# Kernel optimization log

Measured on AMD Instinct MI355X. Metric: run time of the kernel, lower is better.

Reference implementation:

```python
import jax, jax.numpy as jnp
import numpy as np

B, S, D, H = 4, 2048, 1024, 16
DK = D // H

def setup_inputs() -> dict:
    key = jax.random.key(0)
    ks = jax.random.split(key, 12)
    s = 1.0 / np.sqrt(D)
    inp = {
        'q': jax.random.normal(ks[0], (B, S, D), dtype=jnp.float32),
        'k': jax.random.normal(ks[1], (B, S, D), dtype=jnp.float32),
        'v': jax.random.normal(ks[2], (B, S, D), dtype=jnp.float32),
        'mask': jnp.ones((1, 1, S, S), dtype=jnp.int32),
        'w_q': jax.random.normal(ks[3], (D, D), dtype=jnp.float32) * s,
        'b_q': jax.random.normal(ks[4], (D,), dtype=jnp.float32) * s,
        'w_k': jax.random.normal(ks[5], (D, D), dtype=jnp.float32) * s,
        'b_k': jax.random.normal(ks[6], (D,), dtype=jnp.float32) * s,
        'w_v': jax.random.normal(ks[7], (D, D), dtype=jnp.float32) * s,
        'b_v': jax.random.normal(ks[8], (D,), dtype=jnp.float32) * s,
        'w_o': jax.random.normal(ks[9], (D, D), dtype=jnp.float32) * s,
        'b_o': jax.random.normal(ks[10], (D,), dtype=jnp.float32) * s,
    }
    return inp

def reference(q, k, v, mask, w_q, b_q, w_k, b_k, w_v, b_v, w_o, b_o):
    # Linear projections (torch nn.Linear: x @ W^T + b)
    query = q @ w_q.T + b_q            # [B,S,D]
    key_  = k @ w_k.T + b_k
    value = v @ w_v.T + b_v
    # split heads -> [B,H,S,DK]
    def split(x):
        return x.reshape(B, S, H, DK).transpose(0, 2, 1, 3)
    qh, kh, vh = split(query), split(key_), split(value)
    # scaled dot-product attention with full score matrix (naive, faithful)
    scores = jnp.einsum('bhqd,bhkd->bhqk', qh, kh) / jnp.sqrt(jnp.float32(DK))
    scores = jnp.where(mask == 0, jnp.float32(-1e9), scores)
    attn = jax.nn.softmax(scores, axis=-1)  # dropout p=0.0 -> identity
    out = jnp.einsum('bhqk,bhkd->bhqd', attn, vh)
    out = out.transpose(0, 2, 1, 3).reshape(B, S, D)
    return out @ w_o.T + b_o
```

## Files before the change

kernel.cpp:

```cpp
#include <hip/hip_runtime.h>
#include <hip/hip_bf16.h>

typedef __hip_bfloat16 bf16;
typedef __attribute__((ext_vector_type(8))) short bf16x8;
typedef __attribute__((ext_vector_type(4))) float f32x4;

#define GLD16(g, l) __builtin_amdgcn_global_load_lds( \
    (const __attribute__((address_space(1))) void*)(g), \
    (__attribute__((address_space(3))) void*)(l), 16, 0, 0)

__device__ __forceinline__ int xcd_swz(int bid, int cpx) {
  return (bid & 7) * cpx + (bid >> 3);
}


__global__ __launch_bounds__(256) void cvt_all_k(
    const float* __restrict__ q, const float* __restrict__ k,
    const float* __restrict__ v, const float* __restrict__ wq,
    const float* __restrict__ wk, const float* __restrict__ wv,
    const float* __restrict__ wo,
    bf16* __restrict__ qb, bf16* __restrict__ kb, bf16* __restrict__ vb,
    bf16* __restrict__ wqb, bf16* __restrict__ wkb, bf16* __restrict__ wvb,
    bf16* __restrict__ wob) {
  const int bx = blockIdx.x;
  const float* in;
  bf16* out;
  int idx;
  if (bx < 8192) { in = q; out = qb; idx = bx; }
  else if (bx < 16384) { in = k; out = kb; idx = bx - 8192; }
  else if (bx < 24576) { in = v; out = vb; idx = bx - 16384; }
  else {
    const int r = bx - 24576, sel = r >> 10;
    idx = r & 1023;
    in = sel == 0 ? wq : sel == 1 ? wk : sel == 2 ? wv : wo;
    out = sel == 0 ? wqb : sel == 1 ? wkb : sel == 2 ? wvb : wob;
  }
  long i = ((long)idx * 256 + threadIdx.x) * 4;
  float4 vv = *reinterpret_cast<const float4*>(in + i);
  struct alignas(8) B4 { bf16 a, b, c, d; } o;
  o.a = __float2bfloat16(vv.x);
  o.b = __float2bfloat16(vv.y);
  o.c = __float2bfloat16(vv.z);
  o.d = __float2bfloat16(vv.w);
  *reinterpret_cast<B4*>(out + i) = o;
}

template <int MODE>
__global__ __launch_bounds__(512) void gemm_bt_k(
    const bf16* __restrict__ A, const bf16* __restrict__ BT,
    const float* __restrict__ bias, void* __restrict__ outp) {
  __shared__ __align__(16) bf16 As[4][128 * 32];
  __shared__ __align__(16) bf16 Bs[4][128 * 32];
  const int swz = xcd_swz(blockIdx.x, 64);
  const int by = swz >> 3, bx = swz & 7;
  const int t = threadIdx.x;
  const int m0 = by * 128, n0 = bx * 128;
  const int w = t >> 6, lane = t & 63, lr = lane & 15, lg = lane >> 4;
  const int wr = (w >> 1) * 32, wc = (w & 1) * 64;
  f32x4 acc[2][4] = {};
  const int sr = t >> 2;
  const int scol = ((t & 3) ^ (sr & 3)) * 8;
  const bf16* ga = A + (long)(m0 + sr) * 1024 + scol;
  const bf16* gb = BT + (long)(n0 + sr) * 1024 + scol;
#define ISSUE_TILE(itv, buf) do { \
    const int _k = (itv) * 32; \
    GLD16(ga + _k, As[buf] + t * 8); \
    GLD16(gb + _k, Bs[buf] + t * 8); \
  } while (0)
  ISSUE_TILE(0, 0);
  ISSUE_TILE(1, 1);
  for (int it = 0; it < 32; ++it) {
    if (it < 30) {
      ISSUE_TILE(it + 2, (it + 2) & 3);
      asm volatile("s_waitcnt vmcnt(4)" ::: "memory");
    } else if (it == 30) {
      asm volatile("s_waitcnt vmcnt(2)" ::: "memory");
    } else {
      asm volatile("s_waitcnt vmcnt(0)" ::: "memory");
    }
    __builtin_amdgcn_s_barrier();
    const bf16* a_cur = As[it & 3];
    const bf16* b_cur = Bs[it & 3];
    bf16x8 af[2], bfr[4];
#pragma unroll
    for (int m = 0; m < 2; ++m) {
      const int row = wr + m * 16 + lr;
      af[m] = *(const bf16x8*)&a_cur[row * 32 + ((lg ^ (row & 3)) * 8)];
    }
#pragma unroll
    for (int n = 0; n < 4; ++n) {
      const int row = wc + n * 16 + lr;
      bfr[n] = *(const bf16x8*)&b_cur[row * 32 + ((lg ^ (row & 3)) * 8)];
    }
#pragma unroll
    for (int m = 0; m < 2; ++m)
#pragma unroll
      for (int n = 0; n < 4; ++n)
        acc[m][n] = __builtin_amdgcn_mfma_f32_16x16x32_bf16(af[m], bfr[n], acc[m][n], 0, 0, 0);
  }
#pragma unroll
  for (int n = 0; n < 4; ++n) {
    const int j = n0 + wc + n * 16 + lr;
    const float bj = bias[j];
    const int h = j >> 6, dk = j & 63;
#pragma unroll
    for (int m = 0; m < 2; ++m) {
#pragma unroll
      for (int r = 0; r < 4; ++r) {
        const int i = m0 + wr + m * 16 + lg * 4 + r;
        float vv = acc[m][n][r] + bj;
        if (MODE == 3) {
          ((float*)outp)[(long)i * 1024 + j] = vv;
        } else {
          const int b = i >> 11, s = i & 2047;
          if (MODE == 0) vv *= 0.18033688011112042f;
          const bf16 bv = __float2bfloat16(vv);
          if (MODE == 2)
            ((bf16*)outp)[((long)((b * 16 + h) * 64 + dk) << 11) + s] = bv;
          else
            ((bf16*)outp)[((long)((b * 16 + h) * 2048 + s) << 6) + dk] = bv;
        }
      }
    }
  }
#undef ISSUE_TILE
}

__global__ __launch_bounds__(512, 4) void attn_fwd_k(
    const bf16* __restrict__ Qp, const bf16* __restrict__ Kp,
    const bf16* __restrict__ Vp, bf16* __restrict__ Ao) {
  __shared__ __align__(16) bf16 QP[256 * 64];
  __shared__ __align__(16) bf16 Ks[2][64 * 64];
  __shared__ __align__(16) bf16 Vt[2][64 * 64];
  const int t = threadIdx.x;
  const int w = t >> 6, lane = t & 63, lr = lane & 15, lg = lane >> 4;
  const int swz = xcd_swz(blockIdx.x, 64);
  const int bh = swz >> 3;
  const int q0 = (swz & 7) * 256;
  const long hb = (long)bh * 2048 * 64;
  const int sr = t >> 3;
  const int scol8 = (t & 7) * 8;
  const int swcol = (((t & 7) ^ (sr & 7)) * 8);
  const int qscol = ((t & 7) ^ (sr & 7)) * 8;
#pragma unroll
  for (int i = 0; i < 4; ++i)
    GLD16(Qp + hb + (long)(q0 + i * 64 + sr) * 64 + qscol, QP + i * 4096 + t * 8);
  bf16x8 kreg = *(const bf16x8*)&Kp[hb + (long)sr * 64 + scol8];
  bf16x8 vreg = *(const bf16x8*)&Vp[hb + (long)sr * 2048 + scol8];
  *(bf16x8*)&Ks[0][sr * 64 + swcol] = kreg;
  *(bf16x8*)&Vt[0][sr * 64 + swcol] = vreg;
  __syncthreads();
  int fro0[2], fro1[2];
#pragma unroll
  for (int kk = 0; kk < 2; ++kk) {
    fro0[kk] = (w * 32 + lr) * 64 + (((kk * 4 + lg) ^ (lr & 7)) * 8);
    fro1[kk] = (w * 32 + 16 + lr) * 64 + (((kk * 4 + lg) ^ (lr & 7)) * 8);
  }
  int pwo0[4], pwo1[4];
#pragma unroll
  for (int mt = 0; mt < 4; ++mt) {
    const int cs = (((mt * 2 + (lg >> 1)) ^ (lr & 7)) * 8) + (lg & 1) * 4;
    pwo0[mt] = (w * 32 + lr) * 64 + cs;
    pwo1[mt] = (w * 32 + 16 + lr) * 64 + cs;
  }
  bf16x8 aq0[2], aq1[2];
  aq0[0] = *(const bf16x8*)&QP[fro0[0]];
  aq0[1] = *(const bf16x8*)&QP[fro0[1]];
  aq1[0] = *(const bf16x8*)&QP[fro1[0]];
  aq1[1] = *(const bf16x8*)&QP[fro1[1]];
  bf16x8 ones;
  {
    const short o1 = (short)0x3F80;
    ones = bf16x8{o1, o1, o1, o1, o1, o1, o1, o1};
  }
  f32x4 o0[4] = {}, o1[4] = {};
  f32x4 ol0 = {}, ol1 = {};
  struct alignas(8) P4 { __hip_bfloat162 a, b; };
  const f32x4 minit = {-16.f, -16.f, -16.f, -16.f};
  int cur = 0;
  for (int it = 0; it < 32; ++it) {
    if (it < 31) {
      const int kv1 = (it + 1) * 64;
      kreg = *(const bf16x8*)&Kp[hb + (long)(kv1 + sr) * 64 + scol8];
      vreg = *(const bf16x8*)&Vp[hb + (long)sr * 2048 + kv1 + scol8];
    }
    f32x4 s0[4] = {minit, minit, minit, minit};
    f32x4 s1[4] = {minit, minit, minit, minit};
    __builtin_amdgcn_s_setprio(1);
#pragma unroll
    for (int mt = 0; mt < 4; ++mt) {
      const int row = mt * 16 + lr;
#pragma unroll
      for (int kk = 0; kk < 2; ++kk) {
        bf16x8 bk = *(const bf16x8*)&Ks[cur][row * 64 + (((kk * 4 + lg) ^ (lr & 7)) * 8)];
        s0[mt] = __builtin_amdgcn_mfma_f32_16x16x32_bf16(bk, aq0[kk], s0[mt], 0, 0, 0);
        s1[mt] = __builtin_amdgcn_mfma_f32_16x16x32_bf16(bk, aq1[kk], s1[mt], 0, 0, 0);
      }
    }
    __builtin_amdgcn_s_setprio(0);
#pragma unroll
    for (int mt = 0; mt < 4; ++mt) {
      const float p0 = __builtin_amdgcn_exp2f(s0[mt][0]);
      const float p1 = __builtin_amdgcn_exp2f(s0[mt][1]);
      const float p2 = __builtin_amdgcn_exp2f(s0[mt][2]);
      const float p3 = __builtin_amdgcn_exp2f(s0[mt][3]);
      P4 pk;
      pk.a = __float22bfloat162_rn(make_float2(p0, p1));
      pk.b = __float22bfloat162_rn(make_float2(p2, p3));
      *(P4*)&QP[pwo0[mt]] = pk;
    }
#pragma unroll
    for (int mt = 0; mt < 4; ++mt) {
      const float p0 = __builtin_amdgcn_exp2f(s1[mt][0]);
      const float p1 = __builtin_amdgcn_exp2f(s1[mt][1]);
      const float p2 = __builtin_amdgcn_exp2f(s1[mt][2]);
      const float p3 = __builtin_amdgcn_exp2f(s1[mt][3]);
      P4 pk;
      pk.a = __float22bfloat162_rn(make_float2(p0, p1));
      pk.b = __float22bfloat162_rn(make_float2(p2, p3));
      *(P4*)&QP[pwo1[mt]] = pk;
    }
    __builtin_amdgcn_s_setprio(1);
#pragma unroll
    for (int kk = 0; kk < 2; ++kk) {
      bf16x8 ap0 = *(const bf16x8*)&QP[fro0[kk]];
      bf16x8 ap1 = *(const bf16x8*)&QP[fro1[kk]];
#pragma unroll
      for (int n = 0; n < 4; ++n) {
        const int row = n * 16 + lr;
        bf16x8 bv = *(const bf16x8*)&Vt[cur][row * 64 + (((kk * 4 + lg) ^ (lr & 7)) * 8)];
        o0[n] = __builtin_amdgcn_mfma_f32_16x16x32_bf16(ap0, bv, o0[n], 0, 0, 0);
        o1[n] = __builtin_amdgcn_mfma_f32_16x16x32_bf16(ap1, bv, o1[n], 0, 0, 0);
      }
      ol0 = __builtin_amdgcn_mfma_f32_16x16x32_bf16(ap0, ones, ol0, 0, 0, 0);
      ol1 = __builtin_amdgcn_mfma_f32_16x16x32_bf16(ap1, ones, ol1, 0, 0, 0);
    }
    __builtin_amdgcn_s_setprio(0);
    if (it < 31) {
      *(bf16x8*)&Ks[cur ^ 1][sr * 64 + swcol] = kreg;
      *(bf16x8*)&Vt[cur ^ 1][sr * 64 + swcol] = vreg;
    }
    __syncthreads();
    cur ^= 1;
  }
  const int b = bh >> 4, h = bh & 15;
#pragma unroll
  for (int r = 0; r < 4; ++r) {
    {
      const float inv = 1.0f / ol0[r];
      const int sq = q0 + w * 32 + lg * 4 + r;
      const long rb = ((long)(b * 2048 + sq)) * 1024 + h * 64;
#pragma unroll
      for (int n = 0; n < 4; ++n)
        Ao[rb + n * 16 + lr] = __float2bfloat16(o0[n][r] * inv);
    }
    {
      const float inv = 1.0f / ol1[r];
      const int sq = q0 + w * 32 + 16 + lg * 4 + r;
      const long rb = ((long)(b * 2048 + sq)) * 1024 + h * 64;
#pragma unroll
      for (int n = 0; n < 4; ++n)
        Ao[rb + n * 16 + lr] = __float2bfloat16(o1[n][r] * inv);
    }
  }
}

extern "C" void kernel_launch(void* const* d_in, const int* in_sizes, int n_in,
                              void* d_out, int out_size, void* d_ws, size_t ws_size,
                              hipStream_t stream) {
  const float* q   = (const float*)d_in[0];
  const float* k   = (const float*)d_in[1];
  const float* v   = (const float*)d_in[2];
  const float* w_q = (const float*)d_in[4];
  const float* b_q = (const float*)d_in[5];
  const float* w_k = (const float*)d_in[6];
  const float* b_k = (const float*)d_in[7];
  const float* w_v = (const float*)d_in[8];
  const float* b_v = (const float*)d_in[9];
  const float* w_o = (const float*)d_in[10];
  const float* b_o = (const float*)d_in[11];

  char* ws = (char*)d_ws;
  const size_t SZ_QKV = (size_t)8192 * 1024 * 2;
  const size_t SZ_W   = (size_t)1024 * 1024 * 2;
  bf16* qb  = (bf16*)(ws);
  bf16* kb  = (bf16*)(ws + SZ_QKV);
  bf16* vb  = (bf16*)(ws + 2 * SZ_QKV);
  bf16* wqb = (bf16*)(ws + 3 * SZ_QKV);
  bf16* wkb = (bf16*)(ws + 3 * SZ_QKV + SZ_W);
  bf16* wvb = (bf16*)(ws + 3 * SZ_QKV + 2 * SZ_W);
  bf16* wob = (bf16*)(ws + 3 * SZ_QKV + 3 * SZ_W);
  bf16* Qp  = (bf16*)(ws + 3 * SZ_QKV + 4 * SZ_W);
  bf16* Kp  = (bf16*)(ws + 4 * SZ_QKV + 4 * SZ_W);
  bf16* Vp  = (bf16*)(ws + 5 * SZ_QKV + 4 * SZ_W);
  bf16* Ao  = (bf16*)(ws + 6 * SZ_QKV + 4 * SZ_W);

  cvt_all_k<<<28672, 256, 0, stream>>>(q, k, v, w_q, w_k, w_v, w_o,
                                       qb, kb, vb, wqb, wkb, wvb, wob);

  gemm_bt_k<0><<<512, 512, 0, stream>>>(qb, wqb, b_q, (void*)Qp);
  gemm_bt_k<1><<<512, 512, 0, stream>>>(kb, wkb, b_k, (void*)Kp);
  gemm_bt_k<2><<<512, 512, 0, stream>>>(vb, wvb, b_v, (void*)Vp);

  attn_fwd_k<<<512, 512, 0, stream>>>(Qp, Kp, Vp, Ao);

  gemm_bt_k<3><<<512, 512, 0, stream>>>(Ao, wob, b_o, d_out);
}
```

Baseline: 202.5 us.

## Fuse fp32-to-bf16 activation conversion into projection GEMM A-tile loads

Drops the separate conversion pass for q/k/v activations. The projection GEMMs now read fp32 A directly through registers, convert to bf16 and write swizzled LDS tiles, while the B (weight) tiles keep the async global-to-LDS path. This removes a large round trip of writing and re-reading bf16 copies of the inputs, at the cost of register-staged A loads and a restructured two-buffer A pipeline with a launch-bounds occupancy hint. Only the weights are still converted in a separate kernel.

Result: faster. 183.9 us (median of 3 runs) (-9.2%).

```diff
diff --git a/kernel.cpp b/kernel.cpp
--- a/kernel.cpp
+++ b/kernel.cpp
@@ -13,28 +13,22 @@
   return (bid & 7) * cpx + (bid >> 3);
 }
 
-
-__global__ __launch_bounds__(256) void cvt_all_k(
-    const float* __restrict__ q, const float* __restrict__ k,
-    const float* __restrict__ v, const float* __restrict__ wq,
-    const float* __restrict__ wk, const float* __restrict__ wv,
-    const float* __restrict__ wo,
-    bf16* __restrict__ qb, bf16* __restrict__ kb, bf16* __restrict__ vb,
-    bf16* __restrict__ wqb, bf16* __restrict__ wkb, bf16* __restrict__ wvb,
-    bf16* __restrict__ wob) {
-  const int bx = blockIdx.x;
-  const float* in;
-  bf16* out;
-  int idx;
-  if (bx < 8192) { in = q; out = qb; idx = bx; }
-  else if (bx < 16384) { in = k; out = kb; idx = bx - 8192; }
-  else if (bx < 24576) { in = v; out = vb; idx = bx - 16384; }
-  else {
-    const int r = bx - 24576, sel = r >> 10;
-    idx = r & 1023;
-    in = sel == 0 ? wq : sel == 1 ? wk : sel == 2 ? wv : wo;
-    out = sel == 0 ? wqb : sel == 1 ? wkb : sel == 2 ? wvb : wob;
-  }
+__device__ __forceinline__ short bfb(float f) {
+  bf16 h = __float2bfloat16(f);
+  short s;
+  __builtin_memcpy(&s, &h, 2);
+  return s;
+}
+
+
+__global__ __launch_bounds__(256) void cvt_w_k(
+    const float* __restrict__ wq, const float* __restrict__ wk,
+    const float* __restrict__ wv, const float* __restrict__ wo,
+    bf16* __restrict__ wqb, bf16* __restrict__ wkb,
+    bf16* __restrict__ wvb, bf16* __restrict__ wob) {
+  const int sel = blockIdx.x >> 10, idx = blockIdx.x & 1023;
+  const float* in = sel == 0 ? wq : sel == 1 ? wk : sel == 2 ? wv : wo;
+  bf16* out = sel == 0 ? wqb : sel == 1 ? wkb : sel == 2 ? wvb : wob;
   long i = ((long)idx * 256 + threadIdx.x) * 4;
   float4 vv = *reinterpret_cast<const float4*>(in + i);
   struct alignas(8) B4 { bf16 a, b, c, d; } o;
@@ -46,9 +40,94 @@
 }
 
 template <int MODE>
-__global__ __launch_bounds__(512) void gemm_bt_k(
+__global__ __launch_bounds__(512, 5) void gemm_projf_k(
+    const float* __restrict__ A, const bf16* __restrict__ BT,
+    const float* __restrict__ bias, bf16* __restrict__ outp) {
+  __shared__ __align__(16) bf16 As[2][128 * 32];
+  __shared__ __align__(16) bf16 Bs[4][128 * 32];
+  const int swz = xcd_swz(blockIdx.x, 64);
+  const int by = swz >> 3, bx = swz & 7;
+  const int t = threadIdx.x;
+  const int m0 = by * 128, n0 = bx * 128;
+  const int w = t >> 6, lane = t & 63, lr = lane & 15, lg = lane >> 4;
+  const int wr = (w >> 1) * 32, wc = (w & 1) * 64;
+  f32x4 acc[2][4] = {};
+  const int sr = t >> 2;
+  const int scol = ((t & 3) ^ (sr & 3)) * 8;
+  const bf16* gb = BT + (long)(n0 + sr) * 1024 + scol;
+  const int tr = t >> 2, tc = t & 3;
+  const float* ga = A + (long)(m0 + tr) * 1024 + tc * 8;
+  const int awo = tr * 32 + ((tc ^ (tr & 3)) * 8);
+  float4 a0, a1;
+#define LOAD_A(itv) do { \
+    a0 = *(const float4*)(ga + (itv) * 32); \
+    a1 = *(const float4*)(ga + (itv) * 32 + 4); \
+  } while (0)
+#define WRITE_A(buf) do { \
+    bf16x8 ab = bf16x8{bfb(a0.x), bfb(a0.y), bfb(a0.z), bfb(a0.w), \
+                       bfb(a1.x), bfb(a1.y), bfb(a1.z), bfb(a1.w)}; \
+    *(bf16x8*)&As[buf][awo] = ab; \
+  } while (0)
+#define ISSUE_B(itv, buf) GLD16(gb + (itv) * 32, Bs[buf] + t * 8)
+  LOAD_A(0);
+  WRITE_A(0);
+  ISSUE_B(0, 0);
+  ISSUE_B(1, 1);
+  LOAD_A(1);
+  for (int it = 0; it < 32; ++it) {
+    asm volatile("s_waitcnt vmcnt(3) lgkmcnt(0)" ::: "memory");
+    __builtin_amdgcn_s_barrier();
+    const bf16* a_cur = As[it & 1];
+    const bf16* b_cur = Bs[it & 3];
+    bf16x8 af[2], bfr[4];
+#pragma unroll
+    for (int m = 0; m < 2; ++m) {
+      const int row = wr + m * 16 + lr;
+      af[m] = *(const bf16x8*)&a_cur[row * 32 + ((lg ^ (row & 3)) * 8)];
+    }
+#pragma unroll
+    for (int n = 0; n < 4; ++n) {
+      const int row = wc + n * 16 + lr;
+      bfr[n] = *(const bf16x8*)&b_cur[row * 32 + ((lg ^ (row & 3)) * 8)];
+    }
+#pragma unroll
+    for (int m = 0; m < 2; ++m)
+#pragma unroll
+      for (int n = 0; n < 4; ++n)
+        acc[m][n] = __builtin_amdgcn_mfma_f32_16x16x32_bf16(af[m], bfr[n], acc[m][n], 0, 0, 0);
+    if (it < 30) ISSUE_B(it + 2, (it + 2) & 3);
+    if (it < 31) WRITE_A((it + 1) & 1);
+    if (it < 30) LOAD_A(it + 2);
+  }
+#pragma unroll
+  for (int n = 0; n < 4; ++n) {
+    const int j = n0 + wc + n * 16 + lr;
+    const float bj = bias[j];
+    const int h = j >> 6, dk = j & 63;
+#pragma unroll
+    for (int m = 0; m < 2; ++m) {
+#pragma unroll
+      for (int r = 0; r < 4; ++r) {
+        const int i = m0 + wr + m * 16 + lg * 4 + r;
+        float vv = acc[m][n][r] + bj;
+        const int b = i >> 11, s = i & 2047;
+        if (MODE == 0) vv *= 0.18033688011112042f;
+        const bf16 bv = __float2bfloat16(vv);
+        if (MODE == 2)
+          outp[((long)((b * 16 + h) * 64 + dk) << 11) + s] = bv;
+        else
+          outp[((long)((b * 16 + h) * 2048 + s) << 6) + dk] = bv;
+      }
+    }
+  }
+#undef LOAD_A
+#undef WRITE_A
+#undef ISSUE_B
+}
+
+__global__ __launch_bounds__(512) void gemm_out_k(
     const bf16* __restrict__ A, const bf16* __restrict__ BT,
-    const float* __restrict__ bias, void* __restrict__ outp) {
+    const float* __restrict__ bias, float* __restrict__ outp) {
   __shared__ __align__(16) bf16 As[4][128 * 32];
   __shared__ __align__(16) bf16 Bs[4][128 * 32];
   const int swz = xcd_swz(blockIdx.x, 64);
@@ -102,26 +181,13 @@
   for (int n = 0; n < 4; ++n) {
     const int j = n0 + wc + n * 16 + lr;
     const float bj = bias[j];
-    const int h = j >> 6, dk = j & 63;
-#pragma unroll
-    for (int m = 0; m < 2; ++m) {
+#pragma unroll
+    for (int m = 0; m < 2; ++m)
 #pragma unroll
       for (int r = 0; r < 4; ++r) {
         const int i = m0 + wr + m * 16 + lg * 4 + r;
-        float vv = acc[m][n][r] + bj;
-        if (MODE == 3) {
-          ((float*)outp)[(long)i * 1024 + j] = vv;
-        } else {
-          const int b = i >> 11, s = i & 2047;
-          if (MODE == 0) vv *= 0.18033688011112042f;
-          const bf16 bv = __float2bfloat16(vv);
-          if (MODE == 2)
-            ((bf16*)outp)[((long)((b * 16 + h) * 64 + dk) << 11) + s] = bv;
-          else
-            ((bf16*)outp)[((long)((b * 16 + h) * 2048 + s) << 6) + dk] = bv;
-        }
+        outp[(long)i * 1024 + j] = acc[m][n][r] + bj;
       }
-    }
   }
 #undef ISSUE_TILE
 }
@@ -283,26 +349,22 @@
   char* ws = (char*)d_ws;
   const size_t SZ_QKV = (size_t)8192 * 1024 * 2;
   const size_t SZ_W   = (size_t)1024 * 1024 * 2;
-  bf16* qb  = (bf16*)(ws);
-  bf16* kb  = (bf16*)(ws + SZ_QKV);
-  bf16* vb  = (bf16*)(ws + 2 * SZ_QKV);
-  bf16* wqb = (bf16*)(ws + 3 * SZ_QKV);
-  bf16* wkb = (bf16*)(ws + 3 * SZ_QKV + SZ_W);
-  bf16* wvb = (bf16*)(ws + 3 * SZ_QKV + 2 * SZ_W);
-  bf16* wob = (bf16*)(ws + 3 * SZ_QKV + 3 * SZ_W);
-  bf16* Qp  = (bf16*)(ws + 3 * SZ_QKV + 4 * SZ_W);
-  bf16* Kp  = (bf16*)(ws + 4 * SZ_QKV + 4 * SZ_W);
-  bf16* Vp  = (bf16*)(ws + 5 * SZ_QKV + 4 * SZ_W);
-  bf16* Ao  = (bf16*)(ws + 6 * SZ_QKV + 4 * SZ_W);
-
-  cvt_all_k<<<28672, 256, 0, stream>>>(q, k, v, w_q, w_k, w_v, w_o,
-                                       qb, kb, vb, wqb, wkb, wvb, wob);
-
-  gemm_bt_k<0><<<512, 512, 0, stream>>>(qb, wqb, b_q, (void*)Qp);
-  gemm_bt_k<1><<<512, 512, 0, stream>>>(kb, wkb, b_k, (void*)Kp);
-  gemm_bt_k<2><<<512, 512, 0, stream>>>(vb, wvb, b_v, (void*)Vp);
+  bf16* wqb = (bf16*)(ws);
+  bf16* wkb = (bf16*)(ws + SZ_W);
+  bf16* wvb = (bf16*)(ws + 2 * SZ_W);
+  bf16* wob = (bf16*)(ws + 3 * SZ_W);
+  bf16* Qp  = (bf16*)(ws + 4 * SZ_W);
+  bf16* Kp  = (bf16*)(ws + 4 * SZ_W + SZ_QKV);
+  bf16* Vp  = (bf16*)(ws + 4 * SZ_W + 2 * SZ_QKV);
+  bf16* Ao  = (bf16*)(ws + 4 * SZ_W + 3 * SZ_QKV);
+
+  cvt_w_k<<<4096, 256, 0, stream>>>(w_q, w_k, w_v, w_o, wqb, wkb, wvb, wob);
+
+  gemm_projf_k<0><<<512, 512, 0, stream>>>(q, wqb, b_q, Qp);
+  gemm_projf_k<1><<<512, 512, 0, stream>>>(k, wkb, b_k, Kp);
+  gemm_projf_k<2><<<512, 512, 0, stream>>>(v, wvb, b_v, Vp);
 
   attn_fwd_k<<<512, 512, 0, stream>>>(Qp, Kp, Vp, Ao);
 
-  gemm_bt_k<3><<<512, 512, 0, stream>>>(Ao, wob, b_o, d_out);
-}
+  gemm_out_k<<<512, 512, 0, stream>>>(Ao, wob, b_o, (float*)d_out);
+}
```

## Fuse fp32-to-bf16 conversion into GEMM loads, dropping separate convert kernel

Applied to the files above, without the earlier changes.

Removes the standalone conversion kernel that wrote bf16 copies of the inputs and weights. The projection GEMMs now load fp32 directly into registers, convert to bf16 and store to LDS with register double-buffering. The async global-to-LDS loads and 4-stage LDS ring become a 2-stage LDS buffer with a launch-bounds occupancy hint. This saves a full read-write pass over the activations, but GEMM global traffic doubles and the weights are re-converted by every block, with less latency hiding.

After: 188.7 us. 6.8% less time.

```diff
diff --git a/kernel.cpp b/kernel.cpp
--- a/kernel.cpp
+++ b/kernel.cpp
@@ -5,52 +5,28 @@
 typedef __attribute__((ext_vector_type(8))) short bf16x8;
 typedef __attribute__((ext_vector_type(4))) float f32x4;
 
+__device__ __forceinline__ int xcd_swz(int bid, int cpx) {
+  return (bid & 7) * cpx + (bid >> 3);
+}
+
 #define GLD16(g, l) __builtin_amdgcn_global_load_lds( \
     (const __attribute__((address_space(1))) void*)(g), \
     (__attribute__((address_space(3))) void*)(l), 16, 0, 0)
 
-__device__ __forceinline__ int xcd_swz(int bid, int cpx) {
-  return (bid & 7) * cpx + (bid >> 3);
-}
-
-
-__global__ __launch_bounds__(256) void cvt_all_k(
-    const float* __restrict__ q, const float* __restrict__ k,
-    const float* __restrict__ v, const float* __restrict__ wq,
-    const float* __restrict__ wk, const float* __restrict__ wv,
-    const float* __restrict__ wo,
-    bf16* __restrict__ qb, bf16* __restrict__ kb, bf16* __restrict__ vb,
-    bf16* __restrict__ wqb, bf16* __restrict__ wkb, bf16* __restrict__ wvb,
-    bf16* __restrict__ wob) {
-  const int bx = blockIdx.x;
-  const float* in;
-  bf16* out;
-  int idx;
-  if (bx < 8192) { in = q; out = qb; idx = bx; }
-  else if (bx < 16384) { in = k; out = kb; idx = bx - 8192; }
-  else if (bx < 24576) { in = v; out = vb; idx = bx - 16384; }
-  else {
-    const int r = bx - 24576, sel = r >> 10;
-    idx = r & 1023;
-    in = sel == 0 ? wq : sel == 1 ? wk : sel == 2 ? wv : wo;
-    out = sel == 0 ? wqb : sel == 1 ? wkb : sel == 2 ? wvb : wob;
-  }
-  long i = ((long)idx * 256 + threadIdx.x) * 4;
-  float4 vv = *reinterpret_cast<const float4*>(in + i);
-  struct alignas(8) B4 { bf16 a, b, c, d; } o;
-  o.a = __float2bfloat16(vv.x);
-  o.b = __float2bfloat16(vv.y);
-  o.c = __float2bfloat16(vv.z);
-  o.d = __float2bfloat16(vv.w);
-  *reinterpret_cast<B4*>(out + i) = o;
-}
+__device__ __forceinline__ short bfb(float f) {
+  bf16 h = __float2bfloat16(f);
+  short s;
+  __builtin_memcpy(&s, &h, 2);
+  return s;
+}
+
 
 template <int MODE>
-__global__ __launch_bounds__(512) void gemm_bt_k(
-    const bf16* __restrict__ A, const bf16* __restrict__ BT,
+__global__ __launch_bounds__(512, 5) void gemm_f_k(
+    const void* __restrict__ Ap, const float* __restrict__ BTf,
     const float* __restrict__ bias, void* __restrict__ outp) {
-  __shared__ __align__(16) bf16 As[4][128 * 32];
-  __shared__ __align__(16) bf16 Bs[4][128 * 32];
+  __shared__ __align__(16) bf16 As[2][128 * 32];
+  __shared__ __align__(16) bf16 Bs[2][128 * 32];
   const int swz = xcd_swz(blockIdx.x, 64);
   const int by = swz >> 3, bx = swz & 7;
   const int t = threadIdx.x;
@@ -58,29 +34,50 @@
   const int w = t >> 6, lane = t & 63, lr = lane & 15, lg = lane >> 4;
   const int wr = (w >> 1) * 32, wc = (w & 1) * 64;
   f32x4 acc[2][4] = {};
-  const int sr = t >> 2;
-  const int scol = ((t & 3) ^ (sr & 3)) * 8;
-  const bf16* ga = A + (long)(m0 + sr) * 1024 + scol;
-  const bf16* gb = BT + (long)(n0 + sr) * 1024 + scol;
-#define ISSUE_TILE(itv, buf) do { \
-    const int _k = (itv) * 32; \
-    GLD16(ga + _k, As[buf] + t * 8); \
-    GLD16(gb + _k, Bs[buf] + t * 8); \
+  const int tr = t >> 2, tc = t & 3;
+  const int wo = tr * 32 + ((tc ^ (tr & 3)) * 8);
+  const float* gaf = (const float*)Ap + (long)(m0 + tr) * 1024 + tc * 8;
+  const bf16* gab = (const bf16*)Ap + (long)(m0 + tr) * 1024 + tc * 8;
+  const float* gbf = BTf + (long)(n0 + tr) * 1024 + tc * 8;
+  float4 a0, a1, b0, b1;
+  bf16x8 abreg;
+#define LOAD_A(itv) do { \
+    if (MODE != 3) { \
+      a0 = *(const float4*)(gaf + (itv) * 32); \
+      a1 = *(const float4*)(gaf + (itv) * 32 + 4); \
+    } else { \
+      abreg = *(const bf16x8*)(gab + (itv) * 32); \
+    } \
   } while (0)
-  ISSUE_TILE(0, 0);
-  ISSUE_TILE(1, 1);
+#define LOAD_B(itv) do { \
+    b0 = *(const float4*)(gbf + (itv) * 32); \
+    b1 = *(const float4*)(gbf + (itv) * 32 + 4); \
+  } while (0)
+#define WRITE_A(buf) do { \
+    if (MODE != 3) { \
+      bf16x8 ab_ = bf16x8{bfb(a0.x), bfb(a0.y), bfb(a0.z), bfb(a0.w), \
+                          bfb(a1.x), bfb(a1.y), bfb(a1.z), bfb(a1.w)}; \
+      *(bf16x8*)&As[buf][wo] = ab_; \
+    } else { \
+      *(bf16x8*)&As[buf][wo] = abreg; \
+    } \
+  } while (0)
+#define WRITE_B(buf) do { \
+    bf16x8 bb_ = bf16x8{bfb(b0.x), bfb(b0.y), bfb(b0.z), bfb(b0.w), \
+                        bfb(b1.x), bfb(b1.y), bfb(b1.z), bfb(b1.w)}; \
+    *(bf16x8*)&Bs[buf][wo] = bb_; \
+  } while (0)
+  LOAD_A(0);
+  LOAD_B(0);
+  WRITE_A(0);
+  WRITE_B(0);
+  LOAD_A(1);
+  LOAD_B(1);
   for (int it = 0; it < 32; ++it) {
-    if (it < 30) {
-      ISSUE_TILE(it + 2, (it + 2) & 3);
-      asm volatile("s_waitcnt vmcnt(4)" ::: "memory");
-    } else if (it == 30) {
-      asm volatile("s_waitcnt vmcnt(2)" ::: "memory");
-    } else {
-      asm volatile("s_waitcnt vmcnt(0)" ::: "memory");
-    }
+    asm volatile("s_waitcnt lgkmcnt(0)" ::: "memory");
     __builtin_amdgcn_s_barrier();
-    const bf16* a_cur = As[it & 3];
-    const bf16* b_cur = Bs[it & 3];
+    const bf16* a_cur = As[it & 1];
+    const bf16* b_cur = Bs[it & 1];
     bf16x8 af[2], bfr[4];
 #pragma unroll
     for (int m = 0; m < 2; ++m) {
@@ -97,6 +94,14 @@
 #pragma unroll
       for (int n = 0; n < 4; ++n)
         acc[m][n] = __builtin_amdgcn_mfma_f32_16x16x32_bf16(af[m], bfr[n], acc[m][n], 0, 0, 0);
+    if (it < 31) {
+      WRITE_A((it + 1) & 1);
+      WRITE_B((it + 1) & 1);
+    }
+    if (it < 30) {
+      LOAD_A(it + 2);
+      LOAD_B(it + 2);
+    }
   }
 #pragma unroll
   for (int n = 0; n < 4; ++n) {
@@ -123,7 +128,10 @@
       }
     }
   }
-#undef ISSUE_TILE
+#undef LOAD_A
+#undef LOAD_B
+#undef WRITE_A
+#undef WRITE_B
 }
 
 __global__ __launch_bounds__(512, 4) void attn_fwd_k(
@@ -282,27 +290,16 @@
 
   char* ws = (char*)d_ws;
   const size_t SZ_QKV = (size_t)8192 * 1024 * 2;
-  const size_t SZ_W   = (size_t)1024 * 1024 * 2;
-  bf16* qb  = (bf16*)(ws);
-  bf16* kb  = (bf16*)(ws + SZ_QKV);
-  bf16* vb  = (bf16*)(ws + 2 * SZ_QKV);
-  bf16* wqb = (bf16*)(ws + 3 * SZ_QKV);
-  bf16* wkb = (bf16*)(ws + 3 * SZ_QKV + SZ_W);
-  bf16* wvb = (bf16*)(ws + 3 * SZ_QKV + 2 * SZ_W);
-  bf16* wob = (bf16*)(ws + 3 * SZ_QKV + 3 * SZ_W);
-  bf16* Qp  = (bf16*)(ws + 3 * SZ_QKV + 4 * SZ_W);
-  bf16* Kp  = (bf16*)(ws + 4 * SZ_QKV + 4 * SZ_W);
-  bf16* Vp  = (bf16*)(ws + 5 * SZ_QKV + 4 * SZ_W);
-  bf16* Ao  = (bf16*)(ws + 6 * SZ_QKV + 4 * SZ_W);
-
-  cvt_all_k<<<28672, 256, 0, stream>>>(q, k, v, w_q, w_k, w_v, w_o,
-                                       qb, kb, vb, wqb, wkb, wvb, wob);
-
-  gemm_bt_k<0><<<512, 512, 0, stream>>>(qb, wqb, b_q, (void*)Qp);
-  gemm_bt_k<1><<<512, 512, 0, stream>>>(kb, wkb, b_k, (void*)Kp);
-  gemm_bt_k<2><<<512, 512, 0, stream>>>(vb, wvb, b_v, (void*)Vp);
+  bf16* Qp = (bf16*)(ws);
+  bf16* Kp = (bf16*)(ws + SZ_QKV);
+  bf16* Vp = (bf16*)(ws + 2 * SZ_QKV);
+  bf16* Ao = (bf16*)(ws + 3 * SZ_QKV);
+
+  gemm_f_k<0><<<512, 512, 0, stream>>>(q, w_q, b_q, (void*)Qp);
+  gemm_f_k<1><<<512, 512, 0, stream>>>(k, w_k, b_k, (void*)Kp);
+  gemm_f_k<2><<<512, 512, 0, stream>>>(v, w_v, b_v, (void*)Vp);
 
   attn_fwd_k<<<512, 512, 0, stream>>>(Qp, Kp, Vp, Ao);
 
-  gemm_bt_k<3><<<512, 512, 0, stream>>>(Ao, wob, b_o, d_out);
-}
+  gemm_f_k<3><<<512, 512, 0, stream>>>(Ao, w_o, b_o, d_out);
+}
```
